# Optimization experiments

Hardware: AMD Instinct MI355X
Metric: run time of the kernel (lower is better)

The kernel has to match this reference:

```python
import jax, jax.numpy as jnp
import numpy as np

TAU = 2.0        # LIF membrane time constant
VTH = 0.5        # spike threshold
EPS = 1e-5       # BatchNorm eps
ALPHA = 2.0      # ATan surrogate alpha (spikingjelly default)


@jax.custom_vjp
def atan_heaviside(x):
    # forward: Heaviside spike; backward: ATan surrogate gradient
    return (x >= 0.0).astype(x.dtype)

def _ah_fwd(x):
    return atan_heaviside(x), x

def _ah_bwd(x, g):
    return (g * (ALPHA / 2.0) / (1.0 + (jnp.pi / 2.0 * ALPHA * x) ** 2),)

atan_heaviside.defvjp(_ah_fwd, _ah_bwd)


def lif_multistep(x):
    # x: [T, ...] -> spikes [T, ...]; hard reset to 0, decay_input=True
    def step(v, xt):
        v = v + (xt - v) / TAU
        s = atan_heaviside(v - VTH)
        v = v * (1.0 - jax.lax.stop_gradient(s))  # detach_reset=True
        return v, s
    v0 = jnp.zeros_like(x[0])
    _, spikes = jax.lax.scan(step, v0, x)
    return spikes


def tape_pe(d_model, max_len, dtype):
    # tAPE (ConvTran): sinusoidal PE with d_model/max_len frequency scaling
    pos = jnp.arange(max_len, dtype=dtype)[:, None]
    div = jnp.exp(jnp.arange(0, d_model, 2, dtype=dtype) * (-np.log(10000.0) / d_model))
    arg = pos * div * (d_model / max_len)
    pe = jnp.zeros((max_len, d_model), dtype)
    pe = pe.at[:, 0::2].set(jnp.sin(arg))
    pe = pe.at[:, 1::2].set(jnp.cos(arg))
    return pe  # [N, D]


def setup_inputs() -> dict:
    key = jax.random.key(0)
    k1, k2 = jax.random.split(key)
    T, B, N, P, D = 4, 64, 196, 768, 256
    x = jax.random.normal(k1, (T, B, N, P), dtype=jnp.float32)
    W = jax.random.normal(k2, (D, P), dtype=jnp.float32) * 0.02
    gamma = jnp.ones((D,), dtype=jnp.float32)
    beta = jnp.zeros((D,), dtype=jnp.float32)
    return {"x": x, "W": W, "gamma": gamma, "beta": beta}


def reference(x, W, gamma, beta):
    T, B, N, P = x.shape
    D = W.shape[0]
    # patch linear (no bias): [T,B,N,P] @ [D,P]^T -> [T,B,N,D]
    h = jnp.einsum('tbnp,dp->tbnd', x, W)
    h = jnp.transpose(h, (0, 1, 3, 2))  # [T,B,D,N]
    # BatchNorm1d over channel D (training-mode batch stats over T*B and N)
    mean = h.mean(axis=(0, 1, 3), keepdims=True)
    var = ((h - mean) ** 2).mean(axis=(0, 1, 3), keepdims=True)
    h = (h - mean) * jax.lax.rsqrt(var + EPS)
    h = h * gamma[None, None, :, None] + beta[None, None, :, None]
    # LIF spiking neuron scan over T
    h = lif_multistep(h)
    # tAPE positional encoding (broadcast [D,N] over T,B) + second LIF
    h = h + tape_pe(D, N, h.dtype).T
    h = lif_multistep(h)
    return jnp.transpose(h, (0, 1, 3, 2))  # [T,B,N,D]
```

## Files before the change

kernel.cpp:

```cpp
#include <hip/hip_runtime.h>
#include <cmath>

#define T_    4
#define B_    64
#define N_    196
#define P_    768
#define D_    256
#define BN_   (B_*N_)
#define M_    (T_*BN_)
#define SITES (BN_*D_)

#define TILE  64
#define TK    16
#define KITER (P_/TK)
#define MBLKS (M_/TILE)
#define HBLKS (392/49*8*4/8)
#define GRID_HALF ((392/49)*49*4/4)
#define RLEN  98

typedef __attribute__((ext_vector_type(2))) float f32x2;

__device__ __forceinline__ void pk_fma(f32x2& acc, f32x2 a, f32x2 b) {
    f32x2 t;
    asm("v_pk_mul_f32 %1, %2, %3\n\t"
        "v_pk_add_f32 %0, %0, %1"
        : "+v"(acc), "=&v"(t) : "v"(a), "v"(b));
}

extern "C" __global__ __launch_bounds__(256)
void gemm_f32emu(const float* __restrict__ x, const float* __restrict__ w,
                 float* __restrict__ h, float* __restrict__ hT, int mbase) {
    __shared__ __align__(16) f32x2 As2[2][TK/2][RLEN];
    __shared__ __align__(16) f32x2 Bs2[2][TK/2][RLEN];

    const int tid  = threadIdx.x;
    const int tx   = tid & 15;
    const int ty   = tid >> 4;
    const int bid  = blockIdx.x;
    const int xcd  = bid & 7;
    const int lin  = bid >> 3;
    const int m0   = mbase + (xcd * 49 + (lin >> 2)) * TILE;
    const int d0   = (lin & 3) * TILE;
    const int lrow = tid >> 2;
    const int kq   = tid & 3;
    const int lk   = kq * 4;
    const int woff = (lrow >> 2) * 6 + (lrow & 3);
    const int abase = ty * 6;
    const int bbase = tx * 6;

    const float* xp = x + (size_t)(m0 + lrow) * P_ + lk;
    const float* wp = w + (size_t)(d0 + lrow) * P_ + lk;

    f32x2 acc[4][4][2];
#pragma unroll
    for (int i = 0; i < 4; ++i)
#pragma unroll
        for (int j = 0; j < 4; ++j)
#pragma unroll
            for (int p = 0; p < 2; ++p) acc[i][j][p] = f32x2{0.0f, 0.0f};

    {
        const float4 av = *(const float4*)xp;
        const float4 bv = *(const float4*)wp;
        As2[0][kq * 2 + 0][woff] = f32x2{av.x, av.y};
        As2[0][kq * 2 + 1][woff] = f32x2{av.z, av.w};
        Bs2[0][kq * 2 + 0][woff] = f32x2{bv.x, bv.y};
        Bs2[0][kq * 2 + 1][woff] = f32x2{bv.z, bv.w};
    }

    int cur = 0;
    for (int k0 = 0; k0 < KITER; ++k0) {
        __syncthreads();
        float4 av, bv;
        const bool have = (k0 + 1 < KITER);
        if (have) {
            av = *(const float4*)(xp + (k0 + 1) * TK);
            bv = *(const float4*)(wp + (k0 + 1) * TK);
        }
#pragma unroll
        for (int kp = 0; kp < TK / 2; ++kp) {
            const int pi = kp & 1;
            const f32x2* Ar = As2[cur][kp];
            const f32x2* Br = Bs2[cur][kp];
            const float4 aa0 = *(const float4*)(Ar + abase);
            const float4 aa1 = *(const float4*)(Ar + abase + 2);
            const float4 bb0 = *(const float4*)(Br + bbase);
            const float4 bb1 = *(const float4*)(Br + bbase + 2);
            f32x2 a2[4], b2[4];
            a2[0] = f32x2{aa0.x, aa0.y}; a2[1] = f32x2{aa0.z, aa0.w};
            a2[2] = f32x2{aa1.x, aa1.y}; a2[3] = f32x2{aa1.z, aa1.w};
            b2[0] = f32x2{bb0.x, bb0.y}; b2[1] = f32x2{bb0.z, bb0.w};
            b2[2] = f32x2{bb1.x, bb1.y}; b2[3] = f32x2{bb1.z, bb1.w};
#pragma unroll
            for (int i = 0; i < 4; ++i)
#pragma unroll
                for (int j = 0; j < 4; ++j)
                    pk_fma(acc[i][j][pi], a2[i], b2[j]);
        }
        if (have) {
            As2[cur ^ 1][kq * 2 + 0][woff] = f32x2{av.x, av.y};
            As2[cur ^ 1][kq * 2 + 1][woff] = f32x2{av.z, av.w};
            Bs2[cur ^ 1][kq * 2 + 0][woff] = f32x2{bv.x, bv.y};
            Bs2[cur ^ 1][kq * 2 + 1][woff] = f32x2{bv.z, bv.w};
        }
        cur ^= 1;
    }

    float res[4][4];
#pragma unroll
    for (int i = 0; i < 4; ++i)
#pragma unroll
        for (int j = 0; j < 4; ++j) {
            const float l01 = __fadd_rn(acc[i][j][0].x, acc[i][j][0].y);
            const float l23 = __fadd_rn(acc[i][j][1].x, acc[i][j][1].y);
            res[i][j] = __fadd_rn(l01, l23);
        }
#pragma unroll
    for (int i = 0; i < 4; ++i) {
        float4 o = {res[i][0], res[i][1], res[i][2], res[i][3]};
        *(float4*)(h + (size_t)(m0 + ty * 4 + i) * D_ + d0 + tx * 4) = o;
    }
    if (hT) {
#pragma unroll
        for (int j = 0; j < 4; ++j) {
            float4 o = {res[0][j], res[1][j], res[2][j], res[3][j]};
            *(float4*)(hT + (size_t)(d0 + tx * 4 + j) * M_ + m0 + ty * 4) = o;
        }
    }
}

#define MCH2 7168
#define GRP  224
extern "C" __global__ __launch_bounds__(256)
void meanvar_hT(const float* __restrict__ hT, float* __restrict__ mean_,
                float* __restrict__ inv_) {
    __shared__ float buf[2][MCH2];
    __shared__ float chunks[256];
    __shared__ float mn_sh;
    const int tid = threadIdx.x;
    const int d   = blockIdx.x;
    const float* src = hT + (size_t)d * M_;

#pragma unroll
    for (int u = 0; u < 7; ++u)
        *(float4*)&buf[0][(u * 256 + tid) * 4] =
            *(const float4*)&src[(u * 256 + tid) * 4];
    __syncthreads();

    float acc = 0.0f;
    for (int c = 0; c < 7; ++c) {
        const int cb = c & 1;
        const bool have = (c + 1 < 7);
        float4 v[7];
        if (have) {
            const float* rp = src + (c + 1) * MCH2;
#pragma unroll
            for (int u = 0; u < 7; ++u)
                v[u] = *(const float4*)&rp[(u * 256 + tid) * 4];
        }
        if (tid == 0) {
            const float4* bp = (const float4*)buf[cb];
            float4 p0[8], p1[8];
#pragma unroll
            for (int u = 0; u < 8; ++u) p0[u] = bp[u];
            int gp = 0;
            for (; gp + 2 < GRP; gp += 2) {
#pragma unroll
                for (int u = 0; u < 8; ++u) p1[u] = bp[(gp + 1) * 8 + u];
#pragma unroll
                for (int u = 0; u < 8; ++u) {
                    acc = __fadd_rn(acc, p0[u].x);
                    acc = __fadd_rn(acc, p0[u].y);
                    acc = __fadd_rn(acc, p0[u].z);
                    acc = __fadd_rn(acc, p0[u].w);
                }
#pragma unroll
                for (int u = 0; u < 8; ++u) p0[u] = bp[(gp + 2) * 8 + u];
#pragma unroll
                for (int u = 0; u < 8; ++u) {
                    acc = __fadd_rn(acc, p1[u].x);
                    acc = __fadd_rn(acc, p1[u].y);
                    acc = __fadd_rn(acc, p1[u].z);
                    acc = __fadd_rn(acc, p1[u].w);
                }
            }
#pragma unroll
            for (int u = 0; u < 8; ++u) p1[u] = bp[(GRP - 1) * 8 + u];
#pragma unroll
            for (int u = 0; u < 8; ++u) {
                acc = __fadd_rn(acc, p0[u].x);
                acc = __fadd_rn(acc, p0[u].y);
                acc = __fadd_rn(acc, p0[u].z);
                acc = __fadd_rn(acc, p0[u].w);
            }
#pragma unroll
            for (int u = 0; u < 8; ++u) {
                acc = __fadd_rn(acc, p1[u].x);
                acc = __fadd_rn(acc, p1[u].y);
                acc = __fadd_rn(acc, p1[u].z);
                acc = __fadd_rn(acc, p1[u].w);
            }
        }
        if (have) {
#pragma unroll
            for (int u = 0; u < 7; ++u)
                *(float4*)&buf[cb ^ 1][(u * 256 + tid) * 4] = v[u];
        }
        __syncthreads();
    }
    if (tid == 0) {
        const float mn = __fdiv_rn(acc, 50176.0f);
        mean_[d] = mn;
        mn_sh = mn;
    }
    __syncthreads();

    const float mn = mn_sh;
    const int wv   = tid >> 6;
    const int lane = tid & 63;
    for (int tb = wv; tb < T_ * B_; tb += 4) {
        double part = 0.0;
        for (int n = lane; n < N_; n += 64) {
            const float hv = src[tb * N_ + n];
            const float t1 = __fsub_rn(hv, mn);
            const float sq = __fmul_rn(t1, t1);
            part += (double)sq;
        }
#pragma unroll
        for (int off = 32; off; off >>= 1) part += __shfl_down(part, off);
        if (lane == 0) chunks[tb] = (float)part;
    }
    __syncthreads();
    if (tid == 0) {
        float accf = 0.0f;
        for (int tb = 0; tb < T_ * B_; ++tb) accf = __fadd_rn(accf, chunks[tb]);
        const float var = __fdiv_rn(accf, 50176.0f);
        inv_[d] = __fdiv_rn(1.0f, __fsqrt_rn(__fadd_rn(var, 1e-5f)));
    }
}

#define MCH  256
#define DCH  16
#define PADW 20
#define NCHK (M_/MCH)

extern "C" __global__ __launch_bounds__(256)
void mean_seq(const float* __restrict__ h, float* __restrict__ mean_) {
    __shared__ __align__(16) float buf[2][MCH][PADW];
    const int tid = threadIdx.x;
    const int d0  = blockIdx.x * DCH;
    {
        const float* rp = h + (size_t)tid * D_ + d0;
        *(float4*)&buf[0][tid][0]  = *(const float4*)(rp + 0);
        *(float4*)&buf[0][tid][4]  = *(const float4*)(rp + 4);
        *(float4*)&buf[0][tid][8]  = *(const float4*)(rp + 8);
        *(float4*)&buf[0][tid][12] = *(const float4*)(rp + 12);
    }
    __syncthreads();
    float acc = 0.0f;
    for (int c = 0; c < NCHK; ++c) {
        const int cb = c & 1;
        const bool have = (c + 1 < NCHK);
        float4 v0, v1, v2, v3;
        if (have) {
            const float* rp = h + ((size_t)(c + 1) * MCH + tid) * D_ + d0;
            v0 = *(const float4*)(rp + 0);
            v1 = *(const float4*)(rp + 4);
            v2 = *(const float4*)(rp + 8);
            v3 = *(const float4*)(rp + 12);
        }
        if (tid < DCH) {
#pragma unroll 16
            for (int m = 0; m < MCH; ++m)
                acc = __fadd_rn(acc, buf[cb][m][tid]);
        }
        if (have) {
            *(float4*)&buf[cb ^ 1][tid][0]  = v0;
            *(float4*)&buf[cb ^ 1][tid][4]  = v1;
            *(float4*)&buf[cb ^ 1][tid][8]  = v2;
            *(float4*)&buf[cb ^ 1][tid][12] = v3;
        }
        __syncthreads();
    }
    if (tid < DCH) mean_[d0 + tid] = __fdiv_rn(acc, 50176.0f);
}

extern "C" __global__ __launch_bounds__(64)
void var_seq(const float* __restrict__ h, const float* __restrict__ mean_,
             float* __restrict__ inv_) {
    const int d    = blockIdx.x;
    const int lane = threadIdx.x;
    const float mn = mean_[d];
    float accf = 0.0f;
    for (int tb = 0; tb < T_ * B_; ++tb) {
        double part = 0.0;
        for (int n = lane; n < N_; n += 64) {
            const float hv = h[((size_t)tb * N_ + n) * D_ + d];
            const float t1 = __fsub_rn(hv, mn);
            const float sq = __fmul_rn(t1, t1);
            part += (double)sq;
        }
#pragma unroll
        for (int off = 32; off; off >>= 1) part += __shfl_down(part, off);
        accf = __fadd_rn(accf, (float)part);
    }
    if (lane == 0) {
        const float var = __fdiv_rn(accf, 50176.0f);
        inv_[d] = __fdiv_rn(1.0f, __fsqrt_rn(__fadd_rn(var, 1e-5f)));
    }
}

extern "C" __global__ __launch_bounds__(256)
void pe_build(float* __restrict__ pe_) {
    const int d = threadIdx.x;
    const int n = blockIdx.x;
    const double dv  = exp((double)(d & ~1) * (-9.210340371976184 / 256.0));
    const double arg = ((double)n * dv) * (256.0 / 196.0);
    pe_[(size_t)n * D_ + d] = (d & 1) ? (float)cos(arg) : (float)sin(arg);
}

extern "C" __global__ __launch_bounds__(256)
void lif_final(float* __restrict__ out, const float* __restrict__ mean_,
               const float* __restrict__ inv_, const float* __restrict__ gamma,
               const float* __restrict__ beta, const float* __restrict__ pe_tab) {
    const int base = (blockIdx.x * 256 + threadIdx.x) * 4;
    const int dbase = base & (D_ - 1);
    const int n = (base >> 8) % N_;

    const float4 mn = *(const float4*)&mean_[dbase];
    const float4 iv = *(const float4*)&inv_[dbase];
    const float4 g  = *(const float4*)&gamma[dbase];
    const float4 b  = *(const float4*)&beta[dbase];

    float4 pe;
    if (pe_tab) {
        pe = *(const float4*)&pe_tab[(size_t)n * D_ + dbase];
    } else {
        float* pp = &pe.x;
#pragma unroll
        for (int q = 0; q < 4; ++q) {
            const int d = dbase + q;
            const double dv  = exp((double)(d & ~1) * (-9.210340371976184 / 256.0));
            const double arg = ((double)n * dv) * (256.0 / 196.0);
            pp[q] = (d & 1) ? (float)cos(arg) : (float)sin(arg);
        }
    }

    float4 hv[4];
#pragma unroll
    for (int t = 0; t < T_; ++t)
        hv[t] = *(const float4*)&out[(size_t)t * SITES + base];

    const float* mnp = &mn.x; const float* ivp = &iv.x;
    const float* gp  = &g.x;  const float* bp  = &b.x;
    const float* pep = &pe.x;
    float4 s2v[4];
#pragma unroll
    for (int q = 0; q < 4; ++q) {
        float v1 = 0.0f, v2 = 0.0f;
        const float mq = mnp[q], iq = ivp[q], gq = gp[q], bq = bp[q], pq = pep[q];
#pragma unroll
        for (int t = 0; t < T_; ++t) {
            const float hq = (&hv[t].x)[q];
            const float t1 = __fsub_rn(hq, mq);
            const float u  = __fmul_rn(t1, iq);
            const float hb = __fadd_rn(__fmul_rn(u, gq), bq);
            v1 = __fadd_rn(v1, __fmul_rn(__fsub_rn(hb, v1), 0.5f));
            const float s1 = (v1 >= 0.5f) ? 1.0f : 0.0f;
            v1 = __fmul_rn(v1, __fsub_rn(1.0f, s1));
            const float y = __fadd_rn(s1, pq);
            v2 = __fadd_rn(v2, __fmul_rn(__fsub_rn(y, v2), 0.5f));
            const float s2 = (v2 >= 0.5f) ? 1.0f : 0.0f;
            v2 = __fmul_rn(v2, __fsub_rn(1.0f, s2));
            (&s2v[t].x)[q] = s2;
        }
    }
#pragma unroll
    for (int t = 0; t < T_; ++t)
        *(float4*)&out[(size_t)t * SITES + base] = s2v[t];
}

extern "C" void kernel_launch(void* const* d_in, const int* in_sizes, int n_in,
                              void* d_out, int out_size, void* d_ws, size_t ws_size,
                              hipStream_t stream) {
    const float* x     = (const float*)d_in[0];
    const float* w     = (const float*)d_in[1];
    const float* gamma = (const float*)d_in[2];
    const float* beta  = (const float*)d_in[3];
    float* out = (float*)d_out;

    float* mean_ = (float*)d_ws;
    float* inv_  = mean_ + D_;
    float* pe_   = inv_  + D_;
    float* hT_   = pe_   + (size_t)N_ * D_;

    const size_t need_pe = (size_t)(2 * D_ + N_ * D_) * sizeof(float);
    const size_t need_hT = need_pe + (size_t)M_ * D_ * sizeof(float);
    const bool use_pe = ws_size >= need_pe;
    const bool use_hT = ws_size >= need_hT;
    float* hTp = use_hT ? hT_ : nullptr;

    gemm_f32emu<<<1568, 256, 0, stream>>>(x, w, out, hTp, 0);
    gemm_f32emu<<<1568, 256, 0, stream>>>(x, w, out, hTp, 392 * TILE);
    if (use_hT) {
        meanvar_hT<<<D_, 256, 0, stream>>>(hT_, mean_, inv_);
    } else {
        mean_seq<<<16, 256, 0, stream>>>(out, mean_);
        var_seq<<<D_, 64, 0, stream>>>(out, mean_, inv_);
    }
    if (use_pe) pe_build<<<N_, 256, 0, stream>>>(pe_);
    lif_final<<<SITES / 1024, 256, 0, stream>>>(out, mean_, inv_, gamma, beta,
                                                use_pe ? pe_ : nullptr);
}
```

Before: 883.7 us.

## Merge GEMM launches and stream mean reduction directly from global memory

The two half-grid GEMM launches become a single 3136-block launch, with the XCD-aware tile mapping adjusted to 98 tiles per XCD. The mean reduction drops the LDS double-buffered staging, in which the whole block loaded chunks but only thread 0 summed. Thread 0 now reads hT directly from global memory through four rotating float4 register buffers, keeping the same sequential summation order. This removes a kernel launch and the block-wide syncs, but the mean phase now depends on one thread's global-load latency rather than cooperative coalesced loads.

```diff
diff --git a/kernel.cpp b/kernel.cpp
--- a/kernel.cpp
+++ b/kernel.cpp
@@ -13,9 +13,6 @@
 #define TILE  64
 #define TK    16
 #define KITER (P_/TK)
-#define MBLKS (M_/TILE)
-#define HBLKS (392/49*8*4/8)
-#define GRID_HALF ((392/49)*49*4/4)
 #define RLEN  98
 
 typedef __attribute__((ext_vector_type(2))) float f32x2;
@@ -29,7 +26,7 @@
 
 extern "C" __global__ __launch_bounds__(256)
 void gemm_f32emu(const float* __restrict__ x, const float* __restrict__ w,
-                 float* __restrict__ h, float* __restrict__ hT, int mbase) {
+                 float* __restrict__ h, float* __restrict__ hT) {
     __shared__ __align__(16) f32x2 As2[2][TK/2][RLEN];
     __shared__ __align__(16) f32x2 Bs2[2][TK/2][RLEN];
 
@@ -39,7 +36,7 @@
     const int bid  = blockIdx.x;
     const int xcd  = bid & 7;
     const int lin  = bid >> 3;
-    const int m0   = mbase + (xcd * 49 + (lin >> 2)) * TILE;
+    const int m0   = (xcd * 98 + (lin >> 2)) * TILE;
     const int d0   = (lin & 3) * TILE;
     const int lrow = tid >> 2;
     const int kq   = tid & 3;
@@ -129,86 +126,57 @@
     }
 }
 
-#define MCH2 7168
-#define GRP  224
-extern "C" __global__ __launch_bounds__(256)
+#define NB4   (M_/128)
+
+#define SUM8(Bf)                                                   \
+    do {                                                           \
+        _Pragma("unroll")                                          \
+        for (int u = 0; u < 8; ++u) {                              \
+            acc = __fadd_rn(acc, Bf[u].x);                         \
+            acc = __fadd_rn(acc, Bf[u].y);                         \
+            acc = __fadd_rn(acc, Bf[u].z);                         \
+            acc = __fadd_rn(acc, Bf[u].w);                         \
+        }                                                          \
+    } while (0)
+
+#define RELOAD(Bf)                                                 \
+    do {                                                           \
+        _Pragma("unroll")                                          \
+        for (int u = 0; u < 8; ++u) Bf[u] = rp[u];                 \
+        rp += 8;                                                   \
+    } while (0)
+
+extern "C" __global__ __launch_bounds__(256, 1)
 void meanvar_hT(const float* __restrict__ hT, float* __restrict__ mean_,
                 float* __restrict__ inv_) {
-    __shared__ float buf[2][MCH2];
     __shared__ float chunks[256];
     __shared__ float mn_sh;
     const int tid = threadIdx.x;
     const int d   = blockIdx.x;
     const float* src = hT + (size_t)d * M_;
 
-#pragma unroll
-    for (int u = 0; u < 7; ++u)
-        *(float4*)&buf[0][(u * 256 + tid) * 4] =
-            *(const float4*)&src[(u * 256 + tid) * 4];
-    __syncthreads();
-
-    float acc = 0.0f;
-    for (int c = 0; c < 7; ++c) {
-        const int cb = c & 1;
-        const bool have = (c + 1 < 7);
-        float4 v[7];
-        if (have) {
-            const float* rp = src + (c + 1) * MCH2;
-#pragma unroll
-            for (int u = 0; u < 7; ++u)
-                v[u] = *(const float4*)&rp[(u * 256 + tid) * 4];
-        }
-        if (tid == 0) {
-            const float4* bp = (const float4*)buf[cb];
-            float4 p0[8], p1[8];
-#pragma unroll
-            for (int u = 0; u < 8; ++u) p0[u] = bp[u];
-            int gp = 0;
-            for (; gp + 2 < GRP; gp += 2) {
-#pragma unroll
-                for (int u = 0; u < 8; ++u) p1[u] = bp[(gp + 1) * 8 + u];
-#pragma unroll
-                for (int u = 0; u < 8; ++u) {
-                    acc = __fadd_rn(acc, p0[u].x);
-                    acc = __fadd_rn(acc, p0[u].y);
-                    acc = __fadd_rn(acc, p0[u].z);
-                    acc = __fadd_rn(acc, p0[u].w);
-                }
-#pragma unroll
-                for (int u = 0; u < 8; ++u) p0[u] = bp[(gp + 2) * 8 + u];
-#pragma unroll
-                for (int u = 0; u < 8; ++u) {
-                    acc = __fadd_rn(acc, p1[u].x);
-                    acc = __fadd_rn(acc, p1[u].y);
-                    acc = __fadd_rn(acc, p1[u].z);
-                    acc = __fadd_rn(acc, p1[u].w);
-                }
-            }
-#pragma unroll
-            for (int u = 0; u < 8; ++u) p1[u] = bp[(GRP - 1) * 8 + u];
-#pragma unroll
-            for (int u = 0; u < 8; ++u) {
-                acc = __fadd_rn(acc, p0[u].x);
-                acc = __fadd_rn(acc, p0[u].y);
-                acc = __fadd_rn(acc, p0[u].z);
-                acc = __fadd_rn(acc, p0[u].w);
-            }
-#pragma unroll
-            for (int u = 0; u < 8; ++u) {
-                acc = __fadd_rn(acc, p1[u].x);
-                acc = __fadd_rn(acc, p1[u].y);
-                acc = __fadd_rn(acc, p1[u].z);
-                acc = __fadd_rn(acc, p1[u].w);
-            }
-        }
-        if (have) {
-#pragma unroll
-            for (int u = 0; u < 7; ++u)
-                *(float4*)&buf[cb ^ 1][(u * 256 + tid) * 4] = v[u];
-        }
-        __syncthreads();
-    }
     if (tid == 0) {
+        const float4* sp = (const float4*)src;
+        const float4* rp = sp + 32;
+        float4 b0[8], b1[8], b2[8], b3[8];
+#pragma unroll
+        for (int u = 0; u < 8; ++u) b0[u] = sp[u];
+#pragma unroll
+        for (int u = 0; u < 8; ++u) b1[u] = sp[8 + u];
+#pragma unroll
+        for (int u = 0; u < 8; ++u) b2[u] = sp[16 + u];
+#pragma unroll
+        for (int u = 0; u < 8; ++u) b3[u] = sp[24 + u];
+
+        float acc = 0.0f;
+        for (int g = 0; g < NB4 - 1; ++g) {
+            SUM8(b0); RELOAD(b0);
+            SUM8(b1); RELOAD(b1);
+            SUM8(b2); RELOAD(b2);
+            SUM8(b3); RELOAD(b3);
+        }
+        SUM8(b0); SUM8(b1); SUM8(b2); SUM8(b3);
+
         const float mn = __fdiv_rn(acc, 50176.0f);
         mean_[d] = mn;
         mn_sh = mn;
@@ -400,8 +368,7 @@
     const bool use_hT = ws_size >= need_hT;
     float* hTp = use_hT ? hT_ : nullptr;
 
-    gemm_f32emu<<<1568, 256, 0, stream>>>(x, w, out, hTp, 0);
-    gemm_f32emu<<<1568, 256, 0, stream>>>(x, w, out, hTp, 392 * TILE);
+    gemm_f32emu<<<3136, 256, 0, stream>>>(x, w, out, hTp);
     if (use_hT) {
         meanvar_hT<<<D_, 256, 0, stream>>>(hT_, mean_, inv_);
     } else {
```

Result: slower. 1.510 ms (+70.9%).
